# Optimization experiments

Measured on AMD Instinct MI355X. Metric: run time of the kernel, lower is better.

The kernel has to match this reference:

```python
import jax, jax.numpy as jnp
import numpy as np


def setup_inputs() -> dict:
    key = jax.random.key(0)
    ks = jax.random.split(key, 7)
    n, L = 8, 1024
    s = 64            # input_size_1 = input_size_2 = 64
    d = s + 1         # 65, after bias-ones concat / h feature size
    inp = {
        "layer1": jax.random.normal(ks[0], (n, L, s), dtype=jnp.float32),
        "layer2": jax.random.normal(ks[1], (n, L, s), dtype=jnp.float32),
        "layer3": jax.random.normal(ks[2], (n, L, s), dtype=jnp.float32),
        "h1": jax.random.normal(ks[3], (n, L, d), dtype=jnp.float32),
        "h2": jax.random.normal(ks[4], (n, L, d), dtype=jnp.float32),
        "h3": jax.random.normal(ks[5], (n, L, d), dtype=jnp.float32),
        # quartic core W (xavier-normal-ish scale): shape (s1+1, s2+1, s2+1, s2+1)
        "W": jax.random.normal(ks[6], (d, d, d, d), dtype=jnp.float32) * 0.02,
    }
    return inp


def reference(layer1, layer2, layer3, h1, h2, h3, W):
    # Non-factorized, flag=True, 3D-input path of Qriaffine.forward:
    #   out = einsum('nia,abcd,njb,nic,njd->nij', [layer1;1], W, [layer2;1], h1, h2)
    # layer3 / h3 are unused in this branch (but layer3 is still concatenated
    # with ones in the original code, a no-op for the output).
    n, L, _ = layer1.shape
    ones = jnp.ones((n, L, 1), dtype=layer1.dtype)
    l1 = jnp.concatenate([layer1, ones], axis=-1)  # [n, L, d]
    l2 = jnp.concatenate([layer2, ones], axis=-1)  # [n, L, d]
    # efficient contraction order, avoiding the huge [n,L,d,d,d] intermediate:
    p = l1[..., :, None] * h1[..., None, :]          # niac: [n, L, d, d]
    q = jnp.einsum('niac,abcd->nibd', p, W)          # [n, L, d, d]
    r = l2[..., :, None] * h2[..., None, :]          # njbd: [n, L, d, d]
    out = jnp.einsum('nibd,njbd->nij', q, r)         # [n, L, L]
    return out
```

## Files before the change

kernel.cpp:

```cpp
#include <hip/hip_runtime.h>
#include <hip/hip_bf16.h>


typedef __attribute__((ext_vector_type(8))) short short8;
typedef __attribute__((ext_vector_type(16))) float floatx16;

#define KP 4288
#define DP 4352
#define NROW 8192

__device__ __forceinline__ void async_ld16(const void* g, void* l) {
  __builtin_amdgcn_global_load_lds(
      (const __attribute__((address_space(1))) unsigned int*)g,
      (__attribute__((address_space(3))) unsigned int*)l, 16, 0, 0);
}

__global__ void zero_kernel(float4* __restrict__ p, long n) {
  long i = (long)blockIdx.x * blockDim.x + threadIdx.x;
  long stride = (long)gridDim.x * blockDim.x;
  float4 z = make_float4(0.f, 0.f, 0.f, 0.f);
  for (; i < n; i += stride) p[i] = z;
}

__global__ void build_wt2(const float* __restrict__ W, __hip_bfloat16* __restrict__ Wt2) {
  __shared__ __hip_bfloat16 tile[65 * 66];
  const int a = blockIdx.x, b = blockIdx.y;
  const float* src = W + (size_t)(a * 65 + b) * 4225;
  for (int idx = threadIdx.x; idx < 4225; idx += 256) {
    int c = idx / 65, d = idx - c * 65;
    tile[d * 66 + c] = __float2bfloat16(src[idx]);
  }
  __syncthreads();
  for (int idx = threadIdx.x; idx < 4225; idx += 256) {
    int d = idx / 65, c = idx - d * 65;
    Wt2[(size_t)(b * 65 + d) * KP + a * 65 + c] = tile[d * 66 + c];
  }
}

__global__ void build_p(const float* __restrict__ layer, const float* __restrict__ h,
                        __hip_bfloat16* __restrict__ P, int width) {
  const int row = blockIdx.x;
  __shared__ float lv[65], hv[65];
  if (threadIdx.x < 64) lv[threadIdx.x] = layer[(size_t)row * 64 + threadIdx.x];
  if (threadIdx.x == 64) lv[64] = 1.0f;
  if (threadIdx.x < 65) hv[threadIdx.x] = h[(size_t)row * 65 + threadIdx.x];
  __syncthreads();
  for (int base = threadIdx.x * 8; base < width; base += 256 * 8) {
    alignas(16) __hip_bfloat16 tmp[8];
#pragma unroll
    for (int j = 0; j < 8; ++j) {
      int idx = base + j;
      float v = 0.f;
      if (idx < 4225) {
        int x = idx / 65, y = idx - x * 65;
        v = lv[x] * hv[y];
      }
      tmp[j] = __float2bfloat16(v);
    }
    *(float4*)(P + (size_t)row * width + base) = *(const float4*)tmp;
  }
}

template <int STORE_BF16>
__global__ __launch_bounds__(256) void gemm_nt(
    const __hip_bfloat16* __restrict__ A, const __hip_bfloat16* __restrict__ B,
    void* __restrict__ Cv, int K, int lda, int ldb, int ldc,
    long sA, long sB, long sC) {
  __shared__ alignas(16) __hip_bfloat16 As[128 * 64];
  __shared__ alignas(16) __hip_bfloat16 Bs[128 * 64];
  const int z = blockIdx.z;
  A += (long)z * sA;
  B += (long)z * sB;
  const int bm = blockIdx.y * 128;
  const int bn = blockIdx.x * 128;
  const int t = threadIdx.x;
  const int lane = t & 63;
  const int wave = t >> 6;
  const int l31 = lane & 31;
  const int lhi = lane >> 5;
  const int wm = (wave >> 1) * 64;
  const int wn = (wave & 1) * 64;

  const __hip_bfloat16* gA[4];
  const __hip_bfloat16* gB[4];
  __hip_bfloat16* lA[4];
  __hip_bfloat16* lB[4];
#pragma unroll
  for (int r = 0; r < 4; ++r) {
    int L = r * 256 + t;
    int row = L >> 3, sl = L & 7;
    int sg = sl ^ (row & 7);
    gA[r] = A + (size_t)(bm + row) * lda + sg * 8;
    gB[r] = B + (size_t)(bn + row) * ldb + sg * 8;
    lA[r] = As + (size_t)(r * 256 + wave * 64) * 8;
    lB[r] = Bs + (size_t)(r * 256 + wave * 64) * 8;
  }

  const int x7 = l31 & 7;
  const int rA0 = (wm + l31) * 64, rA1 = (wm + 32 + l31) * 64;
  const int rB0 = (wn + l31) * 64, rB1 = (wn + 32 + l31) * 64;

  floatx16 acc[2][2] = {};

  for (int k0 = 0; k0 < K; k0 += 64) {
    __syncthreads();
#pragma unroll
    for (int r = 0; r < 4; ++r) {
      async_ld16(gA[r] + k0, lA[r]);
      async_ld16(gB[r] + k0, lB[r]);
    }
    __syncthreads();

#pragma unroll
    for (int ks = 0; ks < 4; ++ks) {
      const int pc = ((ks * 2 + lhi) ^ x7) * 8;
      short8 a0 = *(const short8*)(&As[rA0 + pc]);
      short8 a1 = *(const short8*)(&As[rA1 + pc]);
      short8 b0 = *(const short8*)(&Bs[rB0 + pc]);
      short8 b1 = *(const short8*)(&Bs[rB1 + pc]);
      acc[0][0] = __builtin_amdgcn_mfma_f32_32x32x16_bf16(a0, b0, acc[0][0], 0, 0, 0);
      acc[0][1] = __builtin_amdgcn_mfma_f32_32x32x16_bf16(a0, b1, acc[0][1], 0, 0, 0);
      acc[1][0] = __builtin_amdgcn_mfma_f32_32x32x16_bf16(a1, b0, acc[1][0], 0, 0, 0);
      acc[1][1] = __builtin_amdgcn_mfma_f32_32x32x16_bf16(a1, b1, acc[1][1], 0, 0, 0);
    }
  }

  if (STORE_BF16) {
    __hip_bfloat16* C = (__hip_bfloat16*)Cv + (long)z * sC;
#pragma unroll
    for (int mt = 0; mt < 2; ++mt)
#pragma unroll
      for (int nt = 0; nt < 2; ++nt)
#pragma unroll
        for (int reg = 0; reg < 16; ++reg) {
          int row = bm + wm + mt * 32 + (reg & 3) + 8 * (reg >> 2) + 4 * lhi;
          int col = bn + wn + nt * 32 + l31;
          C[(size_t)row * ldc + col] = __float2bfloat16(acc[mt][nt][reg]);
        }
  } else {
    float* C = (float*)Cv + (long)z * sC;
#pragma unroll
    for (int mt = 0; mt < 2; ++mt)
#pragma unroll
      for (int nt = 0; nt < 2; ++nt)
#pragma unroll
        for (int reg = 0; reg < 16; ++reg) {
          int row = bm + wm + mt * 32 + (reg & 3) + 8 * (reg >> 2) + 4 * lhi;
          int col = bn + wn + nt * 32 + l31;
          C[(size_t)row * ldc + col] = acc[mt][nt][reg];
        }
  }
}

extern "C" void kernel_launch(void* const* d_in, const int* in_sizes, int n_in,
                              void* d_out, int out_size, void* d_ws, size_t ws_size,
                              hipStream_t stream) {
  const float* layer1 = (const float*)d_in[0];
  const float* layer2 = (const float*)d_in[1];
  const float* h1 = (const float*)d_in[3];
  const float* h2 = (const float*)d_in[4];
  const float* W = (const float*)d_in[6];
  float* out = (float*)d_out;

  char* ws = (char*)d_ws;
  __hip_bfloat16* P = (__hip_bfloat16*)(ws);
  __hip_bfloat16* Wt2 = (__hip_bfloat16*)(ws + 70254592ULL);
  __hip_bfloat16* Q = (__hip_bfloat16*)(ws + 107577344ULL);
  __hip_bfloat16* R = (__hip_bfloat16*)(ws);

  zero_kernel<<<2048, 256, 0, stream>>>((float4*)Wt2, (long)DP * KP * 2 / 16);
  build_wt2<<<dim3(65, 65), 256, 0, stream>>>(W, Wt2);
  build_p<<<NROW, 256, 0, stream>>>(layer1, h1, P, KP);
  gemm_nt<1><<<dim3(DP / 128, NROW / 128, 1), 256, 0, stream>>>(
      P, Wt2, Q, KP, KP, KP, DP, 0, 0, 0);
  build_p<<<NROW, 256, 0, stream>>>(layer2, h2, R, DP);
  gemm_nt<0><<<dim3(1024 / 128, 1024 / 128, 8), 256, 0, stream>>>(
      Q, R, out, DP, DP, DP, 1024, 1024L * DP, 1024L * DP, 1024L * 1024);
}
```

Before: 609.8 us.

## Use 256x256-tile pipelined GEMM with 4-stage LDS ring for first contraction

Replaces the first big GEMM (P x Wt2, 8192x4352x4288) with a new kernel that uses 256x256 block tiles, 512 threads and a K-step of 32. LDS is a 4-slot ring buffer filled by async global-to-LDS loads issued two k-steps ahead, with a single barrier per step. Each wave computes a 128x64 sub-tile, and MFMAs run at raised scheduling priority. The aim is to hide global memory latency and double the data reuse per LDS byte compared with the old load-then-barrier 128x128 loop. In exchange it needs more accumulator registers, which lowers occupancy, and DP/256 = 17 tiles gives a coarser grid.

```diff
diff --git a/kernel.cpp b/kernel.cpp
--- a/kernel.cpp
+++ b/kernel.cpp
@@ -59,6 +59,107 @@
     }
     *(float4*)(P + (size_t)row * width + base) = *(const float4*)tmp;
   }
+}
+
+__global__ __launch_bounds__(512) void gemm1_256(
+    const __hip_bfloat16* __restrict__ A, const __hip_bfloat16* __restrict__ B,
+    __hip_bfloat16* __restrict__ C, int K, int lda, int ldb, int ldc) {
+  __shared__ alignas(16) __hip_bfloat16 As[4 * 256 * 32];
+  __shared__ alignas(16) __hip_bfloat16 Bs[4 * 256 * 32];
+  const int bn = blockIdx.x * 256;
+  const int bm = blockIdx.y * 256;
+  const int t = threadIdx.x;
+  const int lane = t & 63;
+  const int w = t >> 6;
+  const int l31 = lane & 31;
+  const int lhi = lane >> 5;
+  const int x3 = l31 & 3;
+  const int wm = (w >> 2) * 128;
+  const int wn = (w & 3) * 64;
+
+  const __hip_bfloat16* gA[2];
+  const __hip_bfloat16* gB[2];
+  int ldsOff[2];
+#pragma unroll
+  for (int r = 0; r < 2; ++r) {
+    int L = r * 512 + t;
+    int row = L >> 2, p = L & 3;
+    int c = p ^ (row & 3);
+    gA[r] = A + (size_t)(bm + row) * lda + c * 8;
+    gB[r] = B + (size_t)(bn + row) * ldb + c * 8;
+    ldsOff[r] = r * 4096 + w * 512;
+  }
+
+  int rA[4], rB[2];
+#pragma unroll
+  for (int mf = 0; mf < 4; ++mf) rA[mf] = (wm + mf * 32 + l31) * 32;
+#pragma unroll
+  for (int nf = 0; nf < 2; ++nf) rB[nf] = (wn + nf * 32 + l31) * 32;
+
+  const int NT = K >> 5;
+
+#pragma unroll
+  for (int tt = 0; tt < 2; ++tt) {
+#pragma unroll
+    for (int r = 0; r < 2; ++r) {
+      async_ld16(gA[r] + tt * 32, As + tt * 8192 + ldsOff[r]);
+      async_ld16(gB[r] + tt * 32, Bs + tt * 8192 + ldsOff[r]);
+    }
+  }
+  asm volatile("s_waitcnt vmcnt(4)\n\ts_barrier" ::: "memory");
+
+  floatx16 acc[4][2] = {};
+
+  for (int kt = 0; kt < NT; ++kt) {
+    if (kt + 2 < NT) {
+      const int k0 = (kt + 2) * 32;
+      const int bo = ((kt + 2) & 3) * 8192;
+#pragma unroll
+      for (int r = 0; r < 2; ++r) {
+        async_ld16(gA[r] + k0, As + bo + ldsOff[r]);
+        async_ld16(gB[r] + k0, Bs + bo + ldsOff[r]);
+      }
+      __builtin_amdgcn_sched_barrier(0);
+    }
+    const __hip_bfloat16* Ab = As + (kt & 3) * 8192;
+    const __hip_bfloat16* Bb = Bs + (kt & 3) * 8192;
+    short8 a[4][2], b[2][2];
+#pragma unroll
+    for (int ks = 0; ks < 2; ++ks) {
+      const int pc = ((ks * 2 + lhi) ^ x3) * 8;
+#pragma unroll
+      for (int mf = 0; mf < 4; ++mf) a[mf][ks] = *(const short8*)(Ab + rA[mf] + pc);
+#pragma unroll
+      for (int nf = 0; nf < 2; ++nf) b[nf][ks] = *(const short8*)(Bb + rB[nf] + pc);
+    }
+    __builtin_amdgcn_s_setprio(1);
+#pragma unroll
+    for (int ks = 0; ks < 2; ++ks)
+#pragma unroll
+      for (int mf = 0; mf < 4; ++mf)
+#pragma unroll
+        for (int nf = 0; nf < 2; ++nf)
+          acc[mf][nf] = __builtin_amdgcn_mfma_f32_32x32x16_bf16(
+              a[mf][ks], b[nf][ks], acc[mf][nf], 0, 0, 0);
+    __builtin_amdgcn_s_setprio(0);
+    if (kt + 1 < NT) {
+      if (kt + 2 < NT)
+        asm volatile("s_waitcnt vmcnt(4) lgkmcnt(0)\n\ts_barrier" ::: "memory");
+      else
+        asm volatile("s_waitcnt vmcnt(0) lgkmcnt(0)\n\ts_barrier" ::: "memory");
+    }
+  }
+
+#pragma unroll
+  for (int mf = 0; mf < 4; ++mf)
+#pragma unroll
+    for (int nf = 0; nf < 2; ++nf)
+#pragma unroll
+      for (int reg = 0; reg < 16; ++reg) {
+        int row = bm + wm + mf * 32 + (reg & 3) + 8 * (reg >> 2) + 4 * lhi;
+        int col = bn + wn + nf * 32 + l31;
+        C[(size_t)row * ldc + col] = __float2bfloat16(acc[mf][nf][reg]);
+      }
 }
 
 template <int STORE_BF16>
@@ -171,8 +272,8 @@
   zero_kernel<<<2048, 256, 0, stream>>>((float4*)Wt2, (long)DP * KP * 2 / 16);
   build_wt2<<<dim3(65, 65), 256, 0, stream>>>(W, Wt2);
   build_p<<<NROW, 256, 0, stream>>>(layer1, h1, P, KP);
-  gemm_nt<1><<<dim3(DP / 128, NROW / 128, 1), 256, 0, stream>>>(
-      P, Wt2, Q, KP, KP, KP, DP, 0, 0, 0);
+  gemm1_256<<<dim3(DP / 256, NROW / 256), 512, 0, stream>>>(
+      P, Wt2, Q, KP, KP, KP, DP);
   build_p<<<NROW, 256, 0, stream>>>(layer2, h2, R, DP);
   gemm_nt<0><<<dim3(1024 / 128, 1024 / 128, 8), 256, 0, stream>>>(
       Q, R, out, DP, DP, DP, 1024, 1024L * DP, 1024L * DP, 1024L * 1024);
```

Result: slower. 846.0 us (+38.7%).

## Swizzle GEMM blocks per XCD, zero only Wt2 padding, trim second GEMM K

Applied to the files above, without the earlier changes.

Replaces the full-buffer zeroing of the transposed weight with a kernel that only zeroes the padding rows and columns. Adds an XCD-aware block remapping to the large first GEMM so blocks sharing A/B tiles land on the same chiplet's L2. Shrinks the K extent of the second GEMM to skip columns that are guaranteed zero. The swizzle hardcodes the grid shape, so it adds fragility if the sizes change.

```diff
diff --git a/kernel.cpp b/kernel.cpp
--- a/kernel.cpp
+++ b/kernel.cpp
@@ -15,11 +15,22 @@
       (__attribute__((address_space(3))) unsigned int*)l, 16, 0, 0);
 }
 
-__global__ void zero_kernel(float4* __restrict__ p, long n) {
-  long i = (long)blockIdx.x * blockDim.x + threadIdx.x;
-  long stride = (long)gridDim.x * blockDim.x;
-  float4 z = make_float4(0.f, 0.f, 0.f, 0.f);
-  for (; i < n; i += stride) p[i] = z;
+__global__ void zero_pad_wt2(__hip_bfloat16* __restrict__ Wt2) {
+  const int ROWPAD = 127 * KP;
+  const int COLPAD = 4225 * 63;
+  const int total = ROWPAD + COLPAD;
+  const __hip_bfloat16 z = __float2bfloat16(0.f);
+  for (int id = blockIdx.x * 256 + threadIdx.x; id < total;
+       id += gridDim.x * 256) {
+    if (id < ROWPAD) {
+      int row = 4225 + id / KP, col = id % KP;
+      Wt2[(size_t)row * KP + col] = z;
+    } else {
+      int j = id - ROWPAD;
+      int row = j / 63, col = 4225 + j % 63;
+      Wt2[(size_t)row * KP + col] = z;
+    }
+  }
 }
 
 __global__ void build_wt2(const float* __restrict__ W, __hip_bfloat16* __restrict__ Wt2) {
@@ -61,7 +72,7 @@
   }
 }
 
-template <int STORE_BF16>
+template <int STORE_BF16, int SWZ>
 __global__ __launch_bounds__(256) void gemm_nt(
     const __hip_bfloat16* __restrict__ A, const __hip_bfloat16* __restrict__ B,
     void* __restrict__ Cv, int K, int lda, int ldb, int ldc,
@@ -71,8 +82,18 @@
   const int z = blockIdx.z;
   A += (long)z * sA;
   B += (long)z * sB;
-  const int bm = blockIdx.y * 128;
-  const int bn = blockIdx.x * 128;
+  int bx = blockIdx.x, by = blockIdx.y;
+  if (SWZ) {
+    int orig = blockIdx.x + 34 * blockIdx.y;
+    int xcd = orig & 7;
+    int idx = orig >> 3;
+    int xg = (idx < 216) ? (idx / 72) : 3;
+    int r = idx - xg * 72;
+    bx = xg * 9 + (r >> 3);
+    by = (xcd << 3) + (r & 7);
+  }
+  const int bm = by * 128;
+  const int bn = bx * 128;
   const int t = threadIdx.x;
   const int lane = t & 63;
   const int wave = t >> 6;
@@ -168,12 +189,12 @@
   __hip_bfloat16* Q = (__hip_bfloat16*)(ws + 107577344ULL);
   __hip_bfloat16* R = (__hip_bfloat16*)(ws);
 
-  zero_kernel<<<2048, 256, 0, stream>>>((float4*)Wt2, (long)DP * KP * 2 / 16);
+  zero_pad_wt2<<<1024, 256, 0, stream>>>(Wt2);
   build_wt2<<<dim3(65, 65), 256, 0, stream>>>(W, Wt2);
   build_p<<<NROW, 256, 0, stream>>>(layer1, h1, P, KP);
-  gemm_nt<1><<<dim3(DP / 128, NROW / 128, 1), 256, 0, stream>>>(
+  gemm_nt<1, 1><<<dim3(DP / 128, NROW / 128, 1), 256, 0, stream>>>(
       P, Wt2, Q, KP, KP, KP, DP, 0, 0, 0);
   build_p<<<NROW, 256, 0, stream>>>(layer2, h2, R, DP);
-  gemm_nt<0><<<dim3(1024 / 128, 1024 / 128, 8), 256, 0, stream>>>(
-      Q, R, out, DP, DP, DP, 1024, 1024L * DP, 1024L * DP, 1024L * 1024);
-}
+  gemm_nt<0, 0><<<dim3(1024 / 128, 1024 / 128, 8), 256, 0, stream>>>(
+      Q, R, out, 4288, DP, DP, 1024, 1024L * DP, 1024L * DP, 1024L * 1024);
+}
```

Result: faster. 592.3 us (-2.9%).
